# Performance work log

Measured on AMD Instinct MI355X. Metric: run time of the kernel, lower is better.

The kernel has to match this reference:

```python
import jax, jax.numpy as jnp
import numpy as np

N = 100000   # nodes
E = 1600000  # edges
D = 128      # in_dim
H = 128      # hidden_dim
G = 128      # graphs in batch


def setup_inputs() -> dict:
    key = jax.random.key(0)
    ks = jax.random.split(key, 16)
    inp = {
        "x": jax.random.normal(ks[0], (N, D), dtype=jnp.float32),
        "edge_index": jax.random.randint(ks[1], (2, E), 0, N, dtype=jnp.int32),
        "batch": jnp.sort(jax.random.randint(ks[2], (N,), 0, G, dtype=jnp.int32)),
    }
    dims = [(D, H), (H, H), (H, H)]
    k = 3
    for i, (di, dh) in enumerate(dims):
        inp[f"W1_{i}"] = jax.random.normal(ks[k], (di, dh), jnp.float32) * 0.05; k += 1
        inp[f"b1_{i}"] = jnp.zeros((dh,), jnp.float32)
        inp[f"W2_{i}"] = jax.random.normal(ks[k], (dh, dh), jnp.float32) * 0.05; k += 1
        inp[f"b2_{i}"] = jnp.zeros((dh,), jnp.float32)
    return inp


def _gin_layer(x, edge_index, W1, b1, W2, b2):
    # GINConv, eps=0: h_i = MLP(x_i + sum_{j->i} x_j)
    src, dst = edge_index[0], edge_index[1]
    agg = jax.ops.segment_sum(x[src], dst, num_segments=N)  # [N, d]
    h = x + agg
    h = jnp.maximum(h @ W1 + b1, 0.0)  # dropout = identity (eval)
    return h @ W2 + b2


def reference(x, edge_index, batch,
              W1_0, b1_0, W2_0, b2_0,
              W1_1, b1_1, W2_1, b2_1,
              W1_2, b1_2, W2_2, b2_2):
    params = [(W1_0, b1_0, W2_0, b2_0),
              (W1_1, b1_1, W2_1, b2_1),
              (W1_2, b1_2, W2_2, b2_2)]
    h = x
    for (W1, b1, W2, b2) in params:
        h = _gin_layer(h, edge_index, W1, b1, W2, b2)
    # global_mean_pool over batch indices
    sums = jax.ops.segment_sum(h, batch, num_segments=G)             # [G, H]
    cnts = jax.ops.segment_sum(jnp.ones((N,), h.dtype), batch, num_segments=G)
    return sums / jnp.maximum(cnts, 1.0)[:, None]
```

## Files before the change

### kernel.cpp

```cpp
#include <hip/hip_runtime.h>
#include <stdint.h>

#define NN 100000
#define NE 1600000
#define DD 128
#define NG 128
#define NPX 12500
#define NBS 25

using f32x4  = __attribute__((ext_vector_type(4))) float;
using bf16x8 = __attribute__((ext_vector_type(8))) __bf16;

__device__ __forceinline__ unsigned short f2bf(float f) {
  unsigned int u = __builtin_bit_cast(unsigned int, f);
  u = (u + 0x7FFFu + ((u >> 16) & 1u)) >> 16;
  return (unsigned short)u;
}

__device__ __forceinline__ float2 bfu(unsigned int u) {
  float2 r;
  r.x = __builtin_bit_cast(float, u << 16);
  r.y = __builtin_bit_cast(float, u & 0xffff0000u);
  return r;
}

__device__ __forceinline__ void addu4(float* a, uint4 v) {
  float2 p0 = bfu(v.x), p1 = bfu(v.y), p2 = bfu(v.z), p3 = bfu(v.w);
  a[0] += p0.x; a[1] += p0.y; a[2] += p1.x; a[3] += p1.y;
  a[4] += p2.x; a[5] += p2.y; a[6] += p3.x; a[7] += p3.y;
}

union ABu { uint4 q; bf16x8 v; };

__global__ void k_count(const int* __restrict__ dst, int* __restrict__ deg) {
  int xcd = blockIdx.x & 7;
  int e = (blockIdx.x >> 3) * 256 + threadIdx.x;
  if (e >= NE) return;
  int d = dst[e];
  if ((unsigned)(d - xcd * NPX) < (unsigned)NPX) atomicAdd(&deg[d], 1);
}

__global__ __launch_bounds__(1024) void k_scanA(const int* __restrict__ deg,
                                                int* __restrict__ rowptr,
                                                int* __restrict__ bsum) {
  __shared__ int wsum[16];
  const int tid = threadIdx.x, wid = tid >> 6, lane = tid & 63;
  int idx = blockIdx.x * 4096 + tid * 4;
  int v0 = (idx + 0 < NN) ? deg[idx + 0] : 0;
  int v1 = (idx + 1 < NN) ? deg[idx + 1] : 0;
  int v2 = (idx + 2 < NN) ? deg[idx + 2] : 0;
  int v3 = (idx + 3 < NN) ? deg[idx + 3] : 0;
  int tsum = v0 + v1 + v2 + v3;
  int sc = tsum;
  #pragma unroll
  for (int off = 1; off < 64; off <<= 1) {
    int n = __shfl_up(sc, off);
    if (lane >= off) sc += n;
  }
  if (lane == 63) wsum[wid] = sc;
  __syncthreads();
  if (wid == 0 && lane < 16) {
    int w = wsum[lane];
    #pragma unroll
    for (int off = 1; off < 16; off <<= 1) {
      int n = __shfl_up(w, off);
      if (lane >= off) w += n;
    }
    wsum[lane] = w;
  }
  __syncthreads();
  int excl = (wid ? wsum[wid - 1] : 0) + sc - tsum;
  if (idx     <= NN) rowptr[idx]     = excl;
  if (idx + 1 <= NN) rowptr[idx + 1] = excl + v0;
  if (idx + 2 <= NN) rowptr[idx + 2] = excl + v0 + v1;
  if (idx + 3 <= NN) rowptr[idx + 3] = excl + v0 + v1 + v2;
  if (tid == 1023) bsum[blockIdx.x] = wsum[15];
}

__global__ void k_scanB(int* __restrict__ bsum) {
  int lane = threadIdx.x & 63;
  int v = (lane < NBS) ? bsum[lane] : 0;
  int sc = v;
  #pragma unroll
  for (int off = 1; off < 64; off <<= 1) {
    int n = __shfl_up(sc, off);
    if (lane >= off) sc += n;
  }
  if (lane < NBS) bsum[lane] = sc - v;
}

__global__ __launch_bounds__(1024) void k_scanC(int* __restrict__ rowptr,
                                                const int* __restrict__ bsum) {
  int add = bsum[blockIdx.x];
  int idx = blockIdx.x * 4096 + threadIdx.x * 4;
  if (idx     <= NN) rowptr[idx]     += add;
  if (idx + 1 <= NN) rowptr[idx + 1] += add;
  if (idx + 2 <= NN) rowptr[idx + 2] += add;
  if (idx + 3 <= NN) rowptr[idx + 3] += add;
}

__global__ void k_fill(const int* __restrict__ src, const int* __restrict__ dst,
                       const int* __restrict__ rowptr, int* __restrict__ cursor,
                       int* __restrict__ csr) {
  int xcd = blockIdx.x & 7;
  int e = (blockIdx.x >> 3) * 256 + threadIdx.x;
  if (e >= NE) return;
  int d = dst[e];
  if ((unsigned)(d - xcd * NPX) < (unsigned)NPX) {
    int pos = rowptr[d] + atomicAdd(&cursor[d], 1);
    csr[pos] = src[e];
  }
}

__global__ void k_wconv(const float* __restrict__ w0, const float* __restrict__ w1,
                        const float* __restrict__ w2, const float* __restrict__ w3,
                        const float* __restrict__ w4, const float* __restrict__ w5,
                        unsigned short* __restrict__ wt) {
  int idx = blockIdx.x * 256 + threadIdx.x;
  if (idx >= 6 * 16384) return;
  int m = idx >> 14, rem = idx & 16383;
  int n = rem >> 7, k = rem & 127;
  const float* W = (m == 0) ? w0 : (m == 1) ? w1 : (m == 2) ? w2
                 : (m == 3) ? w3 : (m == 4) ? w4 : w5;
  wt[idx] = f2bf(W[k * 128 + n]);
}

__global__ void k_xconv(const float* __restrict__ x, unsigned short* __restrict__ xb) {
  int i = blockIdx.x * 256 + threadIdx.x;
  if (i >= NN * DD / 4) return;
  float4 v = ((const float4*)x)[i];
  uint2 p;
  p.x = (unsigned int)f2bf(v.x) | ((unsigned int)f2bf(v.y) << 16);
  p.y = (unsigned int)f2bf(v.z) | ((unsigned int)f2bf(v.w) << 16);
  ((uint2*)xb)[i] = p;
}

__global__ __launch_bounds__(256) void k_gin(const unsigned short* __restrict__ hb,
                                             const int* __restrict__ rowptr,
                                             const int* __restrict__ csr,
                                             const unsigned short* __restrict__ w1t,
                                             const float* __restrict__ b1,
                                             const unsigned short* __restrict__ w2t,
                                             const float* __restrict__ b2,
                                             unsigned short* __restrict__ hout) {
  __shared__ unsigned short wt_[16 * DD];
  const int wv   = threadIdx.x >> 6;
  const int lane = threadIdx.x & 63;
  const int r16  = lane & 15;
  const int kg   = lane >> 4;
  const int blockBase = blockIdx.x * 16;
  const uint4* h4 = (const uint4*)hb;

  {
    const int lrow = wv * 4 + kg;
    const int node = blockBase + lrow;
    float acc[8] = {0.f,0.f,0.f,0.f,0.f,0.f,0.f,0.f};
    if (node < NN) {
      addu4(acc, h4[(size_t)node * 16 + r16]);
      int j = rowptr[node];
      const int je = rowptr[node + 1];
      for (; j + 7 < je; j += 8) {
        int s0 = csr[j],     s1 = csr[j + 1], s2 = csr[j + 2], s3 = csr[j + 3];
        int s4 = csr[j + 4], s5 = csr[j + 5], s6 = csr[j + 6], s7 = csr[j + 7];
        uint4 v0 = h4[(size_t)s0 * 16 + r16];
        uint4 v1 = h4[(size_t)s1 * 16 + r16];
        uint4 v2 = h4[(size_t)s2 * 16 + r16];
        uint4 v3 = h4[(size_t)s3 * 16 + r16];
        uint4 v4 = h4[(size_t)s4 * 16 + r16];
        uint4 v5 = h4[(size_t)s5 * 16 + r16];
        uint4 v6 = h4[(size_t)s6 * 16 + r16];
        uint4 v7 = h4[(size_t)s7 * 16 + r16];
        addu4(acc, v0); addu4(acc, v1); addu4(acc, v2); addu4(acc, v3);
        addu4(acc, v4); addu4(acc, v5); addu4(acc, v6); addu4(acc, v7);
      }
      for (; j + 3 < je; j += 4) {
        int s0 = csr[j], s1 = csr[j + 1], s2 = csr[j + 2], s3 = csr[j + 3];
        uint4 v0 = h4[(size_t)s0 * 16 + r16];
        uint4 v1 = h4[(size_t)s1 * 16 + r16];
        uint4 v2 = h4[(size_t)s2 * 16 + r16];
        uint4 v3 = h4[(size_t)s3 * 16 + r16];
        addu4(acc, v0); addu4(acc, v1); addu4(acc, v2); addu4(acc, v3);
      }
      for (; j < je; ++j) addu4(acc, h4[(size_t)csr[j] * 16 + r16]);
    }
    uint4 p;
    p.x = (unsigned int)f2bf(acc[0]) | ((unsigned int)f2bf(acc[1]) << 16);
    p.y = (unsigned int)f2bf(acc[2]) | ((unsigned int)f2bf(acc[3]) << 16);
    p.z = (unsigned int)f2bf(acc[4]) | ((unsigned int)f2bf(acc[5]) << 16);
    p.w = (unsigned int)f2bf(acc[6]) | ((unsigned int)f2bf(acc[7]) << 16);
    *(uint4*)(wt_ + lrow * DD + ((r16 ^ (lrow & 7)) << 3)) = p;
  }
  __syncthreads();

  f32x4 acc[2];
  acc[0] = (f32x4){0.f, 0.f, 0.f, 0.f};
  acc[1] = (f32x4){0.f, 0.f, 0.f, 0.f};
  #pragma unroll
  for (int s = 0; s < 4; ++s) {
    ABu au;
    au.q = *(const uint4*)(wt_ + r16 * DD + ((((s << 2) + kg) ^ (r16 & 7)) << 3));
    #pragma unroll
    for (int q = 0; q < 2; ++q) {
      int nb = wv * 2 + q;
      ABu bu; bu.q = *(const uint4*)(w1t + (nb * 16 + r16) * DD + s * 32 + kg * 8);
      acc[q] = __builtin_amdgcn_mfma_f32_16x16x32_bf16(au.v, bu.v, acc[q], 0, 0, 0);
    }
  }
  __syncthreads();
  #pragma unroll
  for (int q = 0; q < 2; ++q) {
    int nb = wv * 2 + q;
    int n = nb * 16 + r16;
    float bias = b1[n];
    #pragma unroll
    for (int reg = 0; reg < 4; ++reg) {
      int urow = (kg << 2) + reg;
      float v = acc[q][reg] + bias;
      v = v > 0.f ? v : 0.f;
      wt_[urow * DD + ((((n >> 3) ^ (urow & 7)) << 3) | (n & 7))] = f2bf(v);
    }
  }
  __syncthreads();

  acc[0] = (f32x4){0.f, 0.f, 0.f, 0.f};
  acc[1] = (f32x4){0.f, 0.f, 0.f, 0.f};
  #pragma unroll
  for (int s = 0; s < 4; ++s) {
    ABu au;
    au.q = *(const uint4*)(wt_ + r16 * DD + ((((s << 2) + kg) ^ (r16 & 7)) << 3));
    #pragma unroll
    for (int q = 0; q < 2; ++q) {
      int nb = wv * 2 + q;
      ABu bu; bu.q = *(const uint4*)(w2t + (nb * 16 + r16) * DD + s * 32 + kg * 8);
      acc[q] = __builtin_amdgcn_mfma_f32_16x16x32_bf16(au.v, bu.v, acc[q], 0, 0, 0);
    }
  }
  #pragma unroll
  for (int reg = 0; reg < 4; ++reg) {
    int row = blockBase + (kg << 2) + reg;
    if (row < NN) {
      #pragma unroll
      for (int q = 0; q < 2; ++q) {
        int n = (wv * 2 + q) * 16 + r16;
        hout[row * DD + n] = f2bf(acc[q][reg] + b2[n]);
      }
    }
  }
}

__global__ __launch_bounds__(256) void k_pool(const unsigned short* __restrict__ hb,
                                              const int* __restrict__ batch,
                                              float* __restrict__ out) {
  const int g  = blockIdx.x;
  const int f2 = threadIdx.x & 63;
  const int rp = threadIdx.x >> 6;
  int lo = 0, hi = NN;
  while (lo < hi) { int m = (lo + hi) >> 1; if (batch[m] < g) lo = m + 1; else hi = m; }
  const int start = lo;
  hi = NN;
  while (lo < hi) { int m = (lo + hi) >> 1; if (batch[m] < g + 1) lo = m + 1; else hi = m; }
  const int end = lo;

  const unsigned int* h32 = (const unsigned int*)hb;
  float2 acc = {0.f, 0.f};
  int i = start + rp;
  for (; i + 4 < end; i += 8) {
    float2 a = bfu(h32[(size_t)i * 64 + f2]);
    float2 b = bfu(h32[(size_t)(i + 4) * 64 + f2]);
    acc.x += a.x + b.x; acc.y += a.y + b.y;
  }
  for (; i < end; i += 4) {
    float2 a = bfu(h32[(size_t)i * 64 + f2]);
    acc.x += a.x; acc.y += a.y;
  }

  __shared__ float2 part[4][64];
  part[rp][f2] = acc;
  __syncthreads();
  if (rp == 0) {
    float2 t0 = part[0][f2], t1 = part[1][f2], t2 = part[2][f2], t3 = part[3][f2];
    float inv = 1.0f / (float)max(end - start, 1);
    out[g * DD + 2 * f2]     = (t0.x + t1.x + t2.x + t3.x) * inv;
    out[g * DD + 2 * f2 + 1] = (t0.y + t1.y + t2.y + t3.y) * inv;
  }
}

extern "C" void kernel_launch(void* const* d_in, const int* in_sizes, int n_in,
                              void* d_out, int out_size, void* d_ws, size_t ws_size,
                              hipStream_t stream) {
  const float* x    = (const float*)d_in[0];
  const int* ei     = (const int*)d_in[1];
  const int* src    = ei;
  const int* dst    = ei + NE;
  const int* batch  = (const int*)d_in[2];

  char* ws = (char*)d_ws;
  size_t off = 0;
  auto alloc = [&](size_t bytes) { char* p = ws + off; off = (off + bytes + 255) & ~(size_t)255; return p; };

  int*  deg    = (int*)alloc(2 * NN * 4);
  int*  cursor = deg + NN;
  int*  rowptr = (int*)alloc((NN + 1) * 4);
  int*  bsum   = (int*)alloc(NBS * 4);
  int*  csr    = (int*)alloc(NE * 4);
  unsigned short* wt = (unsigned short*)alloc(6 * 16384 * 2);
  unsigned short* xb = (unsigned short*)alloc((size_t)NN * DD * 2);
  unsigned short* hA = (unsigned short*)alloc((size_t)NN * DD * 2);
  unsigned short* hB = (unsigned short*)alloc((size_t)NN * DD * 2);

  hipMemsetAsync(deg, 0, 2 * NN * 4, stream);

  k_wconv<<<(6 * 16384 + 255) / 256, 256, 0, stream>>>(
      (const float*)d_in[3], (const float*)d_in[5],
      (const float*)d_in[7], (const float*)d_in[9],
      (const float*)d_in[11], (const float*)d_in[13], wt);
  k_xconv<<<(NN * DD / 4 + 255) / 256, 256, 0, stream>>>(x, xb);

  const int echunks = (NE + 255) / 256;
  k_count<<<8 * echunks, 256, 0, stream>>>(dst, deg);
  k_scanA<<<NBS, 1024, 0, stream>>>(deg, rowptr, bsum);
  k_scanB<<<1, 64, 0, stream>>>(bsum);
  k_scanC<<<NBS, 1024, 0, stream>>>(rowptr, bsum);
  k_fill<<<8 * echunks, 256, 0, stream>>>(src, dst, rowptr, cursor, csr);

  const unsigned short* hin = xb;
  unsigned short* houts[3] = {hA, hB, hA};
  for (int l = 0; l < 3; ++l) {
    k_gin<<<(NN + 15) / 16, 256, 0, stream>>>(
        hin, rowptr, csr,
        wt + (2 * l) * 16384, (const float*)d_in[4 + 4 * l],
        wt + (2 * l + 1) * 16384, (const float*)d_in[6 + 4 * l], houts[l]);
    hin = houts[l];
  }

  k_pool<<<NG, 256, 0, stream>>>(hin, batch, (float*)d_out);
}
```

Measured before the change: 589.0 us.

## Assign one wavefront per node in GIN gather with 1024-thread blocks

The gather phase now uses a full 64-lane wavefront per destination node, each lane loading one 32-bit pair of bf16 features, instead of 16 lanes loading 128-bit chunks. Blocks grow to 1024 threads so 16 waves cover the 16-node tile, and only 8 waves do the two MFMA stages, one 16-column block each. Bounds checks are dropped because NN divides evenly by 16. The aim is more gather parallelism and memory-level parallelism per node. In exchange, loads are narrower, half the waves sit idle during the matmuls, and large blocks may limit occupancy.

```diff
diff --git a/kernel.cpp b/kernel.cpp
--- a/kernel.cpp
+++ b/kernel.cpp
@@ -22,12 +22,6 @@
   r.x = __builtin_bit_cast(float, u << 16);
   r.y = __builtin_bit_cast(float, u & 0xffff0000u);
   return r;
-}
-
-__device__ __forceinline__ void addu4(float* a, uint4 v) {
-  float2 p0 = bfu(v.x), p1 = bfu(v.y), p2 = bfu(v.z), p3 = bfu(v.w);
-  a[0] += p0.x; a[1] += p0.y; a[2] += p1.x; a[3] += p1.y;
-  a[4] += p2.x; a[5] += p2.y; a[6] += p3.x; a[7] += p3.y;
 }
 
 union ABu { uint4 q; bf16x8 v; };
@@ -135,115 +129,93 @@
   ((uint2*)xb)[i] = p;
 }
 
-__global__ __launch_bounds__(256) void k_gin(const unsigned short* __restrict__ hb,
-                                             const int* __restrict__ rowptr,
-                                             const int* __restrict__ csr,
-                                             const unsigned short* __restrict__ w1t,
-                                             const float* __restrict__ b1,
-                                             const unsigned short* __restrict__ w2t,
-                                             const float* __restrict__ b2,
-                                             unsigned short* __restrict__ hout) {
-  __shared__ unsigned short wt_[16 * DD];
+__global__ __launch_bounds__(1024) void k_gin(const unsigned short* __restrict__ hb,
+                                              const int* __restrict__ rowptr,
+                                              const int* __restrict__ csr,
+                                              const unsigned short* __restrict__ w1t,
+                                              const float* __restrict__ b1,
+                                              const unsigned short* __restrict__ w2t,
+                                              const float* __restrict__ b2,
+                                              unsigned short* __restrict__ hout) {
+  __shared__ unsigned short tile[16 * DD];
   const int wv   = threadIdx.x >> 6;
   const int lane = threadIdx.x & 63;
-  const int r16  = lane & 15;
-  const int kg   = lane >> 4;
   const int blockBase = blockIdx.x * 16;
-  const uint4* h4 = (const uint4*)hb;
+  const unsigned int* h32 = (const unsigned int*)hb;
+  unsigned int* t32 = (unsigned int*)tile;
 
   {
-    const int lrow = wv * 4 + kg;
-    const int node = blockBase + lrow;
-    float acc[8] = {0.f,0.f,0.f,0.f,0.f,0.f,0.f,0.f};
-    if (node < NN) {
-      addu4(acc, h4[(size_t)node * 16 + r16]);
-      int j = rowptr[node];
-      const int je = rowptr[node + 1];
-      for (; j + 7 < je; j += 8) {
-        int s0 = csr[j],     s1 = csr[j + 1], s2 = csr[j + 2], s3 = csr[j + 3];
-        int s4 = csr[j + 4], s5 = csr[j + 5], s6 = csr[j + 6], s7 = csr[j + 7];
-        uint4 v0 = h4[(size_t)s0 * 16 + r16];
-        uint4 v1 = h4[(size_t)s1 * 16 + r16];
-        uint4 v2 = h4[(size_t)s2 * 16 + r16];
-        uint4 v3 = h4[(size_t)s3 * 16 + r16];
-        uint4 v4 = h4[(size_t)s4 * 16 + r16];
-        uint4 v5 = h4[(size_t)s5 * 16 + r16];
-        uint4 v6 = h4[(size_t)s6 * 16 + r16];
-        uint4 v7 = h4[(size_t)s7 * 16 + r16];
-        addu4(acc, v0); addu4(acc, v1); addu4(acc, v2); addu4(acc, v3);
-        addu4(acc, v4); addu4(acc, v5); addu4(acc, v6); addu4(acc, v7);
-      }
-      for (; j + 3 < je; j += 4) {
-        int s0 = csr[j], s1 = csr[j + 1], s2 = csr[j + 2], s3 = csr[j + 3];
-        uint4 v0 = h4[(size_t)s0 * 16 + r16];
-        uint4 v1 = h4[(size_t)s1 * 16 + r16];
-        uint4 v2 = h4[(size_t)s2 * 16 + r16];
-        uint4 v3 = h4[(size_t)s3 * 16 + r16];
-        addu4(acc, v0); addu4(acc, v1); addu4(acc, v2); addu4(acc, v3);
-      }
-      for (; j < je; ++j) addu4(acc, h4[(size_t)csr[j] * 16 + r16]);
-    }
-    uint4 p;
-    p.x = (unsigned int)f2bf(acc[0]) | ((unsigned int)f2bf(acc[1]) << 16);
-    p.y = (unsigned int)f2bf(acc[2]) | ((unsigned int)f2bf(acc[3]) << 16);
-    p.z = (unsigned int)f2bf(acc[4]) | ((unsigned int)f2bf(acc[5]) << 16);
-    p.w = (unsigned int)f2bf(acc[6]) | ((unsigned int)f2bf(acc[7]) << 16);
-    *(uint4*)(wt_ + lrow * DD + ((r16 ^ (lrow & 7)) << 3)) = p;
-  }
-  __syncthreads();
-
-  f32x4 acc[2];
-  acc[0] = (f32x4){0.f, 0.f, 0.f, 0.f};
-  acc[1] = (f32x4){0.f, 0.f, 0.f, 0.f};
-  #pragma unroll
-  for (int s = 0; s < 4; ++s) {
-    ABu au;
-    au.q = *(const uint4*)(wt_ + r16 * DD + ((((s << 2) + kg) ^ (r16 & 7)) << 3));
-    #pragma unroll
-    for (int q = 0; q < 2; ++q) {
-      int nb = wv * 2 + q;
-      ABu bu; bu.q = *(const uint4*)(w1t + (nb * 16 + r16) * DD + s * 32 + kg * 8);
-      acc[q] = __builtin_amdgcn_mfma_f32_16x16x32_bf16(au.v, bu.v, acc[q], 0, 0, 0);
-    }
-  }
-  __syncthreads();
-  #pragma unroll
-  for (int q = 0; q < 2; ++q) {
-    int nb = wv * 2 + q;
-    int n = nb * 16 + r16;
+    const int node = blockBase + wv;
+    float2 acc = bfu(h32[(size_t)node * 64 + lane]);
+    int j = rowptr[node];
+    const int je = rowptr[node + 1];
+    for (; j + 7 < je; j += 8) {
+      int s0 = csr[j],     s1 = csr[j + 1], s2 = csr[j + 2], s3 = csr[j + 3];
+      int s4 = csr[j + 4], s5 = csr[j + 5], s6 = csr[j + 6], s7 = csr[j + 7];
+      unsigned int v0 = h32[(size_t)s0 * 64 + lane];
+      unsigned int v1 = h32[(size_t)s1 * 64 + lane];
+      unsigned int v2 = h32[(size_t)s2 * 64 + lane];
+      unsigned int v3 = h32[(size_t)s3 * 64 + lane];
+      unsigned int v4 = h32[(size_t)s4 * 64 + lane];
+      unsigned int v5 = h32[(size_t)s5 * 64 + lane];
+      unsigned int v6 = h32[(size_t)s6 * 64 + lane];
+      unsigned int v7 = h32[(size_t)s7 * 64 + lane];
+      float2 a0 = bfu(v0), a1 = bfu(v1), a2 = bfu(v2), a3 = bfu(v3);
+      float2 a4 = bfu(v4), a5 = bfu(v5), a6 = bfu(v6), a7 = bfu(v7);
+      acc.x += ((a0.x + a1.x) + (a2.x + a3.x)) + ((a4.x + a5.x) + (a6.x + a7.x));
+      acc.y += ((a0.y + a1.y) + (a2.y + a3.y)) + ((a4.y + a5.y) + (a6.y + a7.y));
+    }
+    for (; j < je; ++j) {
+      float2 a = bfu(h32[(size_t)csr[j] * 64 + lane]);
+      acc.x += a.x; acc.y += a.y;
+    }
+    unsigned int packed = (unsigned int)f2bf(acc.x) | ((unsigned int)f2bf(acc.y) << 16);
+    int c = lane >> 2;
+    int o = lane & 3;
+    t32[wv * 64 + ((c ^ (wv & 7)) << 2) + o] = packed;
+  }
+  __syncthreads();
+
+  const int r16 = lane & 15;
+  const int kg  = lane >> 4;
+  f32x4 acc1 = (f32x4){0.f, 0.f, 0.f, 0.f};
+  if (wv < 8) {
+    #pragma unroll
+    for (int s = 0; s < 4; ++s) {
+      ABu au;
+      au.q = *(const uint4*)(tile + r16 * DD + ((((s << 2) + kg) ^ (r16 & 7)) << 3));
+      ABu bu; bu.q = *(const uint4*)(w1t + (wv * 16 + r16) * DD + s * 32 + kg * 8);
+      acc1 = __builtin_amdgcn_mfma_f32_16x16x32_bf16(au.v, bu.v, acc1, 0, 0, 0);
+    }
+  }
+  __syncthreads();
+  if (wv < 8) {
+    int n = wv * 16 + r16;
     float bias = b1[n];
     #pragma unroll
     for (int reg = 0; reg < 4; ++reg) {
       int urow = (kg << 2) + reg;
-      float v = acc[q][reg] + bias;
+      float v = acc1[reg] + bias;
       v = v > 0.f ? v : 0.f;
-      wt_[urow * DD + ((((n >> 3) ^ (urow & 7)) << 3) | (n & 7))] = f2bf(v);
-    }
-  }
-  __syncthreads();
-
-  acc[0] = (f32x4){0.f, 0.f, 0.f, 0.f};
-  acc[1] = (f32x4){0.f, 0.f, 0.f, 0.f};
-  #pragma unroll
-  for (int s = 0; s < 4; ++s) {
-    ABu au;
-    au.q = *(const uint4*)(wt_ + r16 * DD + ((((s << 2) + kg) ^ (r16 & 7)) << 3));
-    #pragma unroll
-    for (int q = 0; q < 2; ++q) {
-      int nb = wv * 2 + q;
-      ABu bu; bu.q = *(const uint4*)(w2t + (nb * 16 + r16) * DD + s * 32 + kg * 8);
-      acc[q] = __builtin_amdgcn_mfma_f32_16x16x32_bf16(au.v, bu.v, acc[q], 0, 0, 0);
-    }
-  }
-  #pragma unroll
-  for (int reg = 0; reg < 4; ++reg) {
-    int row = blockBase + (kg << 2) + reg;
-    if (row < NN) {
-      #pragma unroll
-      for (int q = 0; q < 2; ++q) {
-        int n = (wv * 2 + q) * 16 + r16;
-        hout[row * DD + n] = f2bf(acc[q][reg] + b2[n]);
-      }
+      tile[urow * DD + ((((n >> 3) ^ (urow & 7)) << 3) | (n & 7))] = f2bf(v);
+    }
+  }
+  __syncthreads();
+  if (wv < 8) {
+    f32x4 acc2 = (f32x4){0.f, 0.f, 0.f, 0.f};
+    #pragma unroll
+    for (int s = 0; s < 4; ++s) {
+      ABu au;
+      au.q = *(const uint4*)(tile + r16 * DD + ((((s << 2) + kg) ^ (r16 & 7)) << 3));
+      ABu bu; bu.q = *(const uint4*)(w2t + (wv * 16 + r16) * DD + s * 32 + kg * 8);
+      acc2 = __builtin_amdgcn_mfma_f32_16x16x32_bf16(au.v, bu.v, acc2, 0, 0, 0);
+    }
+    int n = wv * 16 + r16;
+    float bias = b2[n];
+    #pragma unroll
+    for (int reg = 0; reg < 4; ++reg) {
+      int row = blockBase + (kg << 2) + reg;
+      hout[row * DD + n] = f2bf(acc2[reg] + bias);
     }
   }
 }
@@ -326,7 +298,7 @@
   const unsigned short* hin = xb;
   unsigned short* houts[3] = {hA, hB, hA};
   for (int l = 0; l < 3; ++l) {
-    k_gin<<<(NN + 15) / 16, 256, 0, stream>>>(
+    k_gin<<<NN / 16, 1024, 0, stream>>>(
         hin, rowptr, csr,
         wt + (2 * l) * 16384, (const float*)d_in[4 + 4 * l],
         wt + (2 * l + 1) * 16384, (const float*)d_in[6 + 4 * l], houts[l]);
```

After: 702.7 us. +19.3%, slower.
